# Kernel tuning notes

Measured on AMD Instinct MI355X. Metric: run time of the kernel, lower is better.

## Reference

```python
import jax, jax.numpy as jnp
import numpy as np

# ---------------- geometry constants (from init_kwargs) ----------------
N_PROJ = 96          # cone-beam projections (batch of 2D BP, views of 3D BP)
A2D    = 96          # 2D parallel angles (= detector rows of cone sinogram)
DET2D  = 192         # 2D detector bins   (= detector cols of cone sinogram)
DS2D   = 1.0         # 2D detector spacing
H = 128
W = 128              # intermediate CB_projection image (geom_2d volume)
Zd = 128
Yd = 128
Xd = 128             # reconstruction volume (geometry.volume_shape)
DSO = 500.0          # source-isocenter distance
DSD = 1000.0         # source-detector distance
DU = 3.5
DV = 3.5             # 3D detector spacing (detector grid == H x W image grid)


def _grad_lastdim(x):
    # torch.gradient(x, dim=-1) with unit spacing: central diffs, one-sided edges
    left = x[..., 1:2] - x[..., 0:1]
    mid = (x[..., 2:] - x[..., :-2]) * 0.5
    right = x[..., -1:] - x[..., -2:-1]
    return jnp.concatenate([left, mid, right], axis=-1)


def _image_grid(h, w):
    ys = jnp.arange(h, dtype=jnp.float32) - (h - 1) / 2.0
    xs = jnp.arange(w, dtype=jnp.float32) - (w - 1) / 2.0
    yg, xg = jnp.meshgrid(ys, xs, indexing='ij')  # [h, w]
    return yg, xg


def _weights_3d():
    # Defrise-Clack intermediate-function weighting: cosine of ray angle,
    # w(x,y) = D / sqrt(D^2 + x^2 + y^2) on the intermediate image grid.
    yg, xg = _image_grid(H, W)
    return DSD / jnp.sqrt(DSD * DSD + xg * xg + yg * yg)


def _bp2d(sino):
    # Pixel-driven 2D parallel backprojection, batched over N.
    # sino: [N, A2D, DET2D] -> [N, H, W]
    yg, xg = _image_grid(H, W)
    th = jnp.arange(A2D, dtype=jnp.float32) * (np.pi / A2D)
    s = jnp.cos(th)[:, None, None] * xg + jnp.sin(th)[:, None, None] * yg  # [A,H,W]
    pos = s / DS2D + (DET2D - 1) / 2.0
    i0 = jnp.floor(pos).astype(jnp.int32)
    f = pos - i0
    i1 = i0 + 1
    w0 = jnp.where((i0 >= 0) & (i0 < DET2D), 1.0 - f, 0.0)
    w1 = jnp.where((i1 >= 0) & (i1 < DET2D), f, 0.0)
    i0c = jnp.clip(i0, 0, DET2D - 1)
    i1c = jnp.clip(i1, 0, DET2D - 1)
    aa = jnp.arange(A2D)[:, None, None]  # [A,1,1]
    g0 = sino[:, aa, i0c]  # [N, A, H, W]
    g1 = sino[:, aa, i1c]
    return (g0 * w0 + g1 * w1).sum(axis=1)  # [N, H, W]


def _bp3d(projs):
    # Voxel-driven circular cone-beam backprojection with FDK distance weight.
    # projs: [N_PROJ, H, W] (V=H rows, U=W cols) -> volume [Zd, Yd, Xd]
    zs = jnp.arange(Zd, dtype=jnp.float32) - (Zd - 1) / 2.0
    ys = jnp.arange(Yd, dtype=jnp.float32) - (Yd - 1) / 2.0
    xs = jnp.arange(Xd, dtype=jnp.float32) - (Xd - 1) / 2.0
    zz, yy, xx = jnp.meshgrid(zs, ys, xs, indexing='ij')  # [Z,Y,X]
    betas = jnp.arange(N_PROJ, dtype=jnp.float32) * (2.0 * np.pi / N_PROJ)

    def body(acc, inp):
        beta, proj = inp
        cb, sb = jnp.cos(beta), jnp.sin(beta)
        t = xx * cb + yy * sb          # along central ray
        s = -xx * sb + yy * cb         # transaxial offset
        r = DSO + t                    # source-to-voxel-plane distance
        pu = (DSD * s / r) / DU + (W - 1) / 2.0
        pv = (DSD * zz / r) / DV + (H - 1) / 2.0
        iu0 = jnp.floor(pu).astype(jnp.int32); fu = pu - iu0; iu1 = iu0 + 1
        iv0 = jnp.floor(pv).astype(jnp.int32); fv = pv - iv0; iv1 = iv0 + 1
        mu0 = (iu0 >= 0) & (iu0 < W); mu1 = (iu1 >= 0) & (iu1 < W)
        mv0 = (iv0 >= 0) & (iv0 < H); mv1 = (iv1 >= 0) & (iv1 < H)
        iu0c = jnp.clip(iu0, 0, W - 1); iu1c = jnp.clip(iu1, 0, W - 1)
        iv0c = jnp.clip(iv0, 0, H - 1); iv1c = jnp.clip(iv1, 0, H - 1)
        w00 = jnp.where(mv0 & mu0, (1 - fv) * (1 - fu), 0.0)
        w01 = jnp.where(mv0 & mu1, (1 - fv) * fu, 0.0)
        w10 = jnp.where(mv1 & mu0, fv * (1 - fu), 0.0)
        w11 = jnp.where(mv1 & mu1, fv * fu, 0.0)
        val = (proj[iv0c, iu0c] * w00 + proj[iv0c, iu1c] * w01 +
               proj[iv1c, iu0c] * w10 + proj[iv1c, iu1c] * w11)
        acc = acc + val * (DSD / r) ** 2
        return acc, None

    acc, _ = jax.lax.scan(body, jnp.zeros((Zd, Yd, Xd), jnp.float32), (betas, projs))
    return acc


def setup_inputs() -> dict:
    key = jax.random.key(0)
    k1, k2 = jax.random.split(key)
    sinogram = jax.random.normal(k1, (1, 1, N_PROJ, A2D, DET2D), dtype=jnp.float32)
    weight = jax.random.uniform(k2, (1, N_PROJ, A2D, DET2D), dtype=jnp.float32)
    prelu_weight = jnp.full((1,), 0.25, dtype=jnp.float32)
    return {"sinogram": sinogram, "weight": weight, "prelu_weight": prelu_weight}


def reference(sinogram, weight, prelu_weight):
    ws = sinogram[0] * weight                 # [1, N, A, D]
    deriv = _grad_lastdim(ws)[0]              # [N, A, D]  (squeeze dim 0)
    cb = _bp2d(deriv)                         # [N, H, W]
    weighted_cb = cb * _weights_3d()          # [N, H, W]
    reco = _bp3d(weighted_cb)[None]           # [1, Z, Y, X]
    a = prelu_weight[0]
    return jnp.where(reco >= 0, reco, a * reco)  # PReLU (single parameter)
```

## Files before the change

### kernel.cpp

```cpp
#include <hip/hip_runtime.h>
#include <hip/hip_fp16.h>
#include <math.h>

#define NPROJ 96
#define NANG  96
#define DET   192
#define NPIX  16384
#define SLICE (NANG*DET)

#define KPROJ 285.7142857142857f

__device__ __forceinline__ float frcp(float x) { return __builtin_amdgcn_rcpf(x); }

__device__ __forceinline__ float ffract(float x) {
#if __has_builtin(__builtin_amdgcn_fractf)
    return __builtin_amdgcn_fractf(x);
#else
    return x - floorf(x);
#endif
}

typedef __fp16 h2 __attribute__((ext_vector_type(2)));

__device__ __forceinline__ unsigned pack2(float a, float b) {
    h2 p = __builtin_amdgcn_cvt_pkrtz(a, b);
    return __builtin_bit_cast(unsigned, p);
}
__device__ __forceinline__ h2 as_h2(unsigned u) { return __builtin_bit_cast(h2, u); }

#if __has_builtin(__builtin_amdgcn_fdot2)
#define FDOT2(a, b, c) __builtin_amdgcn_fdot2((a), (b), (c), false)
#else
__device__ __forceinline__ float FDOT2(h2 a, h2 b, float c) {
    return c + (float)a[0] * (float)b[0] + (float)a[1] * (float)b[1];
}
#endif

__global__ __launch_bounds__(192) void k_deriv(const float* __restrict__ sino,
                                               const float* __restrict__ wgt,
                                               unsigned* __restrict__ derivp) {
    __shared__ float row[DET];
    const int r = blockIdx.x;
    const int d = threadIdx.x;
    const int base = r * DET + d;
    row[d] = sino[base] * wgt[base];
    __syncthreads();
    auto grad = [&](int i) -> float {
        i = (i > DET-1) ? DET-1 : i;
        if (i == 0)       return row[1] - row[0];
        if (i == DET-1)   return row[DET-1] - row[DET-2];
        return 0.5f * (row[i+1] - row[i-1]);
    };
    const float g0 = grad(d), g1 = grad(d+1);
    derivp[base] = pack2(g0, g1 - g0);
}

__global__ __launch_bounds__(256) void k_bp2d(const unsigned* __restrict__ derivp,
                                              unsigned* __restrict__ wq_dw) {
    __shared__ float sc[NANG], ss[NANG];
    __shared__ float buf[512];
    const int p   = blockIdx.x;
    const int tid = threadIdx.x;

    if (tid < NANG) {
        float s_, c_;
        sincosf((float)tid * (float)(3.14159265358979323846 / 96.0), &s_, &c_);
        sc[tid] = c_; ss[tid] = s_;
    }

    const int pixbase = blockIdx.y * 512;
    float acc[2], fx[2], fy[2];
    #pragma unroll
    for (int i = 0; i < 2; ++i) {
        const int pix = pixbase + i*256 + tid;
        fx[i] = (float)(pix & 127) - 63.5f;
        fy[i] = (float)(pix >> 7)  - 63.5f;
        acc[i] = 0.0f;
    }
    __syncthreads();

    const unsigned* rowp = derivp + p * SLICE;
    for (int a = 0; a < NANG; ++a, rowp += DET) {
        const float cb = sc[a], sb = ss[a];
        #pragma unroll
        for (int i = 0; i < 2; ++i) {
            const float pos = fmaf(cb, fx[i], fmaf(sb, fy[i], 95.5f));
            const int   i0  = (int)pos;
            const float f   = ffract(pos);
            acc[i] = FDOT2(as_h2(rowp[i0]), as_h2(pack2(1.0f, f)), acc[i]);
        }
    }

    #pragma unroll
    for (int i = 0; i < 2; ++i) {
        const float w = 1000.0f * rsqrtf(1000000.0f + fx[i]*fx[i] + fy[i]*fy[i]);
        buf[i*256 + tid] = acc[i] * w;
    }
    __syncthreads();

    unsigned* sq = wq_dw + p * (NPIX * 4);
    #pragma unroll
    for (int i = 0; i < 2; ++i) {
        const int l   = i*256 + tid;
        const int pix = pixbase + l;
        const int u   = pix & 127;
        const int v   = pix >> 7;
        const float v0 = buf[l];
        const float v1 = (u < 127) ? buf[l + 1] : 0.0f;
        const unsigned pr = pack2(v0, v1 - v0);
        #pragma unroll
        for (int k = 0; k < 4; ++k) {
            const int vb = v - k;
            if (vb >= 0) sq[(((vb << 7) + u) << 2) + k] = pr;
        }
    }
}

__global__ __launch_bounds__(256) void k_bp3d_q(const uint4* __restrict__ wq,
                                                const float* __restrict__ prelu,
                                                float* __restrict__ out) {
    __shared__ float sc[NPROJ], ss[NPROJ];
    const int tid = threadIdx.x;
    const int x   = tid & 127;
    const int y   = (blockIdx.x << 1) | (tid >> 7);
    const int z0  = blockIdx.y << 2;

    if (tid < NPROJ) {
        float s_, c_;
        sincosf((float)tid * (float)(2.0 * 3.14159265358979323846 / 96.0), &s_, &c_);
        sc[tid] = c_; ss[tid] = s_;
    }

    const float fx  = (float)x - 63.5f;
    const float fy  = (float)y - 63.5f;
    const float zlo = (float)z0 - 63.5f;

    float acc[4];
    #pragma unroll
    for (int j = 0; j < 4; ++j) acc[j] = 0.0f;

    __syncthreads();

    const uint4* bb = wq;
    for (int b = 0; b < NPROJ; ++b, bb += NPIX) {
        const float cb    = sc[b], sb = ss[b];
        const float t     = fmaf(fx, cb,  fy * sb);
        const float sdist = fmaf(fy, cb, -fx * sb);
        const float invr  = frcp(500.0f + t);
        const float pu    = fmaf(KPROJ * sdist, invr, 63.5f);
        const int   iu0   = (int)pu;
        const float fu    = ffract(pu);
        float w2 = 1000.0f * invr; w2 *= w2;
        const float Kz    = KPROJ * invr;
        const h2    wuw   = as_h2(pack2(w2, fu * w2));

        #pragma unroll
        for (int pr2 = 0; pr2 < 2; ++pr2) {
            const float pvA = fmaf(Kz, zlo + (float)(2*pr2), 63.5f);
            const float pvB = pvA + Kz;
            const int   ivA = (int)pvA;
            const int   ivB = (int)pvB;
            const float fvA = ffract(pvA);
            const float fvB = ffract(pvB);
            const uint4 q   = bb[(ivA << 7) + iu0];
            const int   d   = ivB - ivA;
            const float tA  = FDOT2(as_h2(q.x), wuw, 0.0f);
            const float bA  = FDOT2(as_h2(q.y), wuw, 0.0f);
            acc[2*pr2]     += fmaf(fvA, bA - tA, tA);
            const unsigned tBv = d ? q.y : q.x;
            const unsigned bBv = d ? q.z : q.y;
            const float tB  = FDOT2(as_h2(tBv), wuw, 0.0f);
            const float bB  = FDOT2(as_h2(bBv), wuw, 0.0f);
            acc[2*pr2 + 1] += fmaf(fvB, bB - tB, tB);
        }
    }

    const float a = prelu[0];
    #pragma unroll
    for (int j = 0; j < 4; ++j) {
        const float v = acc[j];
        out[((z0 + j) << 14) + (y << 7) + x] = (v >= 0.0f) ? v : a * v;
    }
}

extern "C" void kernel_launch(void* const* d_in, const int* in_sizes, int n_in,
                              void* d_out, int out_size, void* d_ws, size_t ws_size,
                              hipStream_t stream) {
    const float* sino  = (const float*)d_in[0];
    const float* wgt   = (const float*)d_in[1];
    const float* prelu = (const float*)d_in[2];
    float* out = (float*)d_out;

    unsigned* wq_dw  = (unsigned*)d_ws;
    unsigned* derivp = wq_dw + (size_t)NPROJ * NPIX * 4;

    k_deriv<<<dim3(NPROJ * NANG), dim3(192), 0, stream>>>(sino, wgt, derivp);
    k_bp2d <<<dim3(NPROJ, 32),    dim3(256), 0, stream>>>(derivp, wq_dw);
    k_bp3d_q<<<dim3(64, 32),      dim3(256), 0, stream>>>((const uint4*)wq_dw, prelu, out);
}
```

Before: 188.0 us.

## Shrink intermediate to 2-row packed layout and do 8 z-voxels per thread

The bp2d output now stores each pixel's data with only two rows (v, v+1) as a uint2, replacing the 4-row uint4 replication. This halves the intermediate buffer and the bytes written and read. In exchange, bp3d issues two 8-byte gathers per z-pair instead of one 16-byte gather plus selects. Each bp3d thread now accumulates 8 z voxels, which halves the grid and amortizes the per-projection geometry math, at the cost of more registers.

```diff
diff --git a/kernel.cpp b/kernel.cpp
--- a/kernel.cpp
+++ b/kernel.cpp
@@ -98,7 +98,7 @@
     }
     __syncthreads();
 
-    unsigned* sq = wq_dw + p * (NPIX * 4);
+    unsigned* sq = wq_dw + p * (NPIX * 2);
     #pragma unroll
     for (int i = 0; i < 2; ++i) {
         const int l   = i*256 + tid;
@@ -108,22 +108,19 @@
         const float v0 = buf[l];
         const float v1 = (u < 127) ? buf[l + 1] : 0.0f;
         const unsigned pr = pack2(v0, v1 - v0);
-        #pragma unroll
-        for (int k = 0; k < 4; ++k) {
-            const int vb = v - k;
-            if (vb >= 0) sq[(((vb << 7) + u) << 2) + k] = pr;
-        }
+        sq[(((v << 7) + u) << 1)] = pr;
+        if (v >= 1) sq[((((v - 1) << 7) + u) << 1) + 1] = pr;
     }
 }
 
-__global__ __launch_bounds__(256) void k_bp3d_q(const uint4* __restrict__ wq,
+__global__ __launch_bounds__(256) void k_bp3d_p(const uint2* __restrict__ wp,
                                                 const float* __restrict__ prelu,
                                                 float* __restrict__ out) {
     __shared__ float sc[NPROJ], ss[NPROJ];
     const int tid = threadIdx.x;
     const int x   = tid & 127;
     const int y   = (blockIdx.x << 1) | (tid >> 7);
-    const int z0  = blockIdx.y << 2;
+    const int z0  = blockIdx.y << 3;
 
     if (tid < NPROJ) {
         float s_, c_;
@@ -133,16 +130,18 @@
 
     const float fx  = (float)x - 63.5f;
     const float fy  = (float)y - 63.5f;
-    const float zlo = (float)z0 - 63.5f;
+    float za[4];
+    #pragma unroll
+    for (int j = 0; j < 4; ++j) za[j] = (float)z0 - 63.5f + (float)(2*j);
 
-    float acc[4];
+    float acc[8];
     #pragma unroll
-    for (int j = 0; j < 4; ++j) acc[j] = 0.0f;
+    for (int j = 0; j < 8; ++j) acc[j] = 0.0f;
 
     __syncthreads();
 
-    const uint4* bb = wq;
-    for (int b = 0; b < NPROJ; ++b, bb += NPIX) {
+    const char* bbc = (const char*)wp;
+    for (int b = 0; b < NPROJ; ++b, bbc += (size_t)NPIX * sizeof(uint2)) {
         const float cb    = sc[b], sb = ss[b];
         const float t     = fmaf(fx, cb,  fy * sb);
         const float sdist = fmaf(fy, cb, -fx * sb);
@@ -153,31 +152,30 @@
         float w2 = 1000.0f * invr; w2 *= w2;
         const float Kz    = KPROJ * invr;
         const h2    wuw   = as_h2(pack2(w2, fu * w2));
+        const unsigned ub = ((unsigned)iu0) << 3;
 
         #pragma unroll
-        for (int pr2 = 0; pr2 < 2; ++pr2) {
-            const float pvA = fmaf(Kz, zlo + (float)(2*pr2), 63.5f);
+        for (int pr2 = 0; pr2 < 4; ++pr2) {
+            const float pvA = fmaf(Kz, za[pr2], 63.5f);
             const float pvB = pvA + Kz;
             const int   ivA = (int)pvA;
             const int   ivB = (int)pvB;
             const float fvA = ffract(pvA);
             const float fvB = ffract(pvB);
-            const uint4 q   = bb[(ivA << 7) + iu0];
-            const int   d   = ivB - ivA;
-            const float tA  = FDOT2(as_h2(q.x), wuw, 0.0f);
-            const float bA  = FDOT2(as_h2(q.y), wuw, 0.0f);
+            const uint2 qA  = *(const uint2*)(bbc + ((((unsigned)ivA) << 10) + ub));
+            const uint2 qB  = *(const uint2*)(bbc + ((((unsigned)ivB) << 10) + ub));
+            const float tA  = FDOT2(as_h2(qA.x), wuw, 0.0f);
+            const float bA  = FDOT2(as_h2(qA.y), wuw, 0.0f);
             acc[2*pr2]     += fmaf(fvA, bA - tA, tA);
-            const unsigned tBv = d ? q.y : q.x;
-            const unsigned bBv = d ? q.z : q.y;
-            const float tB  = FDOT2(as_h2(tBv), wuw, 0.0f);
-            const float bB  = FDOT2(as_h2(bBv), wuw, 0.0f);
+            const float tB  = FDOT2(as_h2(qB.x), wuw, 0.0f);
+            const float bB  = FDOT2(as_h2(qB.y), wuw, 0.0f);
             acc[2*pr2 + 1] += fmaf(fvB, bB - tB, tB);
         }
     }
 
     const float a = prelu[0];
     #pragma unroll
-    for (int j = 0; j < 4; ++j) {
+    for (int j = 0; j < 8; ++j) {
         const float v = acc[j];
         out[((z0 + j) << 14) + (y << 7) + x] = (v >= 0.0f) ? v : a * v;
     }
@@ -192,9 +190,9 @@
     float* out = (float*)d_out;
 
     unsigned* wq_dw  = (unsigned*)d_ws;
-    unsigned* derivp = wq_dw + (size_t)NPROJ * NPIX * 4;
+    unsigned* derivp = wq_dw + (size_t)NPROJ * NPIX * 2;
 
     k_deriv<<<dim3(NPROJ * NANG), dim3(192), 0, stream>>>(sino, wgt, derivp);
     k_bp2d <<<dim3(NPROJ, 32),    dim3(256), 0, stream>>>(derivp, wq_dw);
-    k_bp3d_q<<<dim3(64, 32),      dim3(256), 0, stream>>>((const uint4*)wq_dw, prelu, out);
+    k_bp3d_p<<<dim3(64, 16),      dim3(256), 0, stream>>>((const uint2*)wq_dw, prelu, out);
 }
```

Measured after the change: 212.0 us. 12.7% more time.

## Precompute per-projection 3D backprojection geometry table and crop unused detector rows

Applied to the files above, without the earlier changes.

The per-(projection, x, y) geometry of the 3D backprojection no longer runs in every z-block. It is now computed once in the 2D backprojection kernel and stored as a packed table holding the fp16 weights, iu0 packed into Kz's low mantissa bits, and Kz. The 3D kernel loads this table with a software prefetch and issues both z-pair gathers up front, so it skips the trig, reciprocal and fract work that was repeated 32 times. The intermediate buffer keeps only detector rows 16..111, which shrinks the writes and the footprint. Trade-offs: an extra 12 MB table read per z-block, a slight loss of Kz precision, and the row crop assumes projections never fall outside that range.

```diff
diff --git a/kernel.cpp b/kernel.cpp
--- a/kernel.cpp
+++ b/kernel.cpp
@@ -7,6 +7,10 @@
 #define DET   192
 #define NPIX  16384
 #define SLICE (NANG*DET)
+
+#define WQROW0   16
+#define WQROWS   96
+#define WQSLICEB (WQROWS*128*16)
 
 #define KPROJ 285.7142857142857f
 
@@ -56,7 +60,8 @@
 }
 
 __global__ __launch_bounds__(256) void k_bp2d(const unsigned* __restrict__ derivp,
-                                              unsigned* __restrict__ wq_dw) {
+                                              unsigned* __restrict__ wq_dw,
+                                              uint2* __restrict__ tbl) {
     __shared__ float sc[NANG], ss[NANG];
     __shared__ float buf[512];
     const int p   = blockIdx.x;
@@ -67,6 +72,9 @@
         sincosf((float)tid * (float)(3.14159265358979323846 / 96.0), &s_, &c_);
         sc[tid] = c_; ss[tid] = s_;
     }
+
+    float sb2, cb2;
+    sincosf((float)p * (float)(2.0 * 3.14159265358979323846 / 96.0), &sb2, &cb2);
 
     const int pixbase = blockIdx.y * 512;
     float acc[2], fx[2], fy[2];
@@ -98,7 +106,8 @@
     }
     __syncthreads();
 
-    unsigned* sq = wq_dw + p * (NPIX * 4);
+    unsigned* sq = wq_dw + p * (WQROWS * 128 * 4);
+    uint2*    tp = tbl   + p * NPIX;
     #pragma unroll
     for (int i = 0; i < 2; ++i) {
         const int l   = i*256 + tid;
@@ -111,68 +120,88 @@
         #pragma unroll
         for (int k = 0; k < 4; ++k) {
             const int vb = v - k;
-            if (vb >= 0) sq[(((vb << 7) + u) << 2) + k] = pr;
-        }
-    }
-}
-
-__global__ __launch_bounds__(256) void k_bp3d_q(const uint4* __restrict__ wq,
-                                                const float* __restrict__ prelu,
-                                                float* __restrict__ out) {
-    __shared__ float sc[NPROJ], ss[NPROJ];
+            if (vb >= WQROW0 && vb < WQROW0 + WQROWS)
+                sq[(((vb - WQROW0) << 7) + u) << 2 | k] = pr;
+        }
+        const float t3   = fmaf(fx[i], cb2,  fy[i] * sb2);
+        const float sd3  = fmaf(fy[i], cb2, -fx[i] * sb2);
+        const float invr = frcp(500.0f + t3);
+        const float pu   = fmaf(KPROJ * sd3, invr, 63.5f);
+        const int   iu0  = (int)pu;
+        const float fu   = ffract(pu);
+        float w2 = 1000.0f * invr; w2 *= w2;
+        const float Kz   = KPROJ * invr;
+        const unsigned kzi = (__builtin_bit_cast(unsigned, Kz) & ~127u) | (unsigned)iu0;
+        uint2 e; e.x = pack2(w2, fu * w2); e.y = kzi;
+        tp[pix] = e;
+    }
+}
+
+__global__ __launch_bounds__(256, 8) void k_bp3d_t(const unsigned char* __restrict__ wq,
+                                                   const uint2* __restrict__ tbl,
+                                                   const float* __restrict__ prelu,
+                                                   float* __restrict__ out) {
     const int tid = threadIdx.x;
     const int x   = tid & 127;
     const int y   = (blockIdx.x << 1) | (tid >> 7);
     const int z0  = blockIdx.y << 2;
-
-    if (tid < NPROJ) {
-        float s_, c_;
-        sincosf((float)tid * (float)(2.0 * 3.14159265358979323846 / 96.0), &s_, &c_);
-        sc[tid] = c_; ss[tid] = s_;
-    }
-
-    const float fx  = (float)x - 63.5f;
-    const float fy  = (float)y - 63.5f;
+    const int pix = (y << 7) + x;
+
     const float zlo = (float)z0 - 63.5f;
 
     float acc[4];
     #pragma unroll
     for (int j = 0; j < 4; ++j) acc[j] = 0.0f;
 
-    __syncthreads();
-
-    const uint4* bb = wq;
-    for (int b = 0; b < NPROJ; ++b, bb += NPIX) {
-        const float cb    = sc[b], sb = ss[b];
-        const float t     = fmaf(fx, cb,  fy * sb);
-        const float sdist = fmaf(fy, cb, -fx * sb);
-        const float invr  = frcp(500.0f + t);
-        const float pu    = fmaf(KPROJ * sdist, invr, 63.5f);
-        const int   iu0   = (int)pu;
-        const float fu    = ffract(pu);
-        float w2 = 1000.0f * invr; w2 *= w2;
-        const float Kz    = KPROJ * invr;
-        const h2    wuw   = as_h2(pack2(w2, fu * w2));
-
-        #pragma unroll
-        for (int pr2 = 0; pr2 < 2; ++pr2) {
-            const float pvA = fmaf(Kz, zlo + (float)(2*pr2), 63.5f);
-            const float pvB = pvA + Kz;
-            const int   ivA = (int)pvA;
-            const int   ivB = (int)pvB;
-            const float fvA = ffract(pvA);
-            const float fvB = ffract(pvB);
-            const uint4 q   = bb[(ivA << 7) + iu0];
-            const int   d   = ivB - ivA;
-            const float tA  = FDOT2(as_h2(q.x), wuw, 0.0f);
-            const float bA  = FDOT2(as_h2(q.y), wuw, 0.0f);
-            acc[2*pr2]     += fmaf(fvA, bA - tA, tA);
-            const unsigned tBv = d ? q.y : q.x;
-            const unsigned bBv = d ? q.z : q.y;
-            const float tB  = FDOT2(as_h2(tBv), wuw, 0.0f);
-            const float bB  = FDOT2(as_h2(bBv), wuw, 0.0f);
-            acc[2*pr2 + 1] += fmaf(fvB, bB - tB, tB);
-        }
+    const uint2* tp = tbl + pix;
+    const unsigned char* sp = wq;
+
+    uint2 Tc = *tp; tp += NPIX;
+
+    for (int b = 0; b < NPROJ; ++b, tp += NPIX, sp += WQSLICEB) {
+        const uint2 Tn = *tp;
+        const h2    wuw = as_h2(Tc.x);
+        const int   iu0 = (int)(Tc.y & 127u);
+        const float Kz  = __builtin_bit_cast(float, Tc.y & ~127u);
+        const int   ub2 = (iu0 << 4) - (WQROW0 << 11);
+
+        const float pvA0 = fmaf(Kz, zlo, 63.5f);
+        const float pvB0 = pvA0 + Kz;
+        const int   ivA0 = (int)pvA0;
+        const int   d0   = (int)pvB0 - ivA0;
+        const float fvA0 = ffract(pvA0);
+        const float fvB0 = ffract(pvB0);
+        const uint4 q0   = *(const uint4*)(sp + ((ivA0 << 11) + ub2));
+
+        const float pvA1 = fmaf(Kz, zlo + 2.0f, 63.5f);
+        const float pvB1 = pvA1 + Kz;
+        const int   ivA1 = (int)pvA1;
+        const int   d1   = (int)pvB1 - ivA1;
+        const float fvA1 = ffract(pvA1);
+        const float fvB1 = ffract(pvB1);
+        const uint4 q1   = *(const uint4*)(sp + ((ivA1 << 11) + ub2));
+
+        {
+            const float tA = FDOT2(as_h2(q0.x), wuw, 0.0f);
+            const float bA = FDOT2(as_h2(q0.y), wuw, 0.0f);
+            acc[0] += fmaf(fvA0, bA - tA, tA);
+            const unsigned tBv = d0 ? q0.y : q0.x;
+            const unsigned bBv = d0 ? q0.z : q0.y;
+            const float tB = FDOT2(as_h2(tBv), wuw, 0.0f);
+            const float bB = FDOT2(as_h2(bBv), wuw, 0.0f);
+            acc[1] += fmaf(fvB0, bB - tB, tB);
+        }
+        {
+            const float tA = FDOT2(as_h2(q1.x), wuw, 0.0f);
+            const float bA = FDOT2(as_h2(q1.y), wuw, 0.0f);
+            acc[2] += fmaf(fvA1, bA - tA, tA);
+            const unsigned tBv = d1 ? q1.y : q1.x;
+            const unsigned bBv = d1 ? q1.z : q1.y;
+            const float tB = FDOT2(as_h2(tBv), wuw, 0.0f);
+            const float bB = FDOT2(as_h2(bBv), wuw, 0.0f);
+            acc[3] += fmaf(fvB1, bB - tB, tB);
+        }
+        Tc = Tn;
     }
 
     const float a = prelu[0];
@@ -191,10 +220,13 @@
     const float* prelu = (const float*)d_in[2];
     float* out = (float*)d_out;
 
-    unsigned* wq_dw  = (unsigned*)d_ws;
-    unsigned* derivp = wq_dw + (size_t)NPROJ * NPIX * 4;
-
-    k_deriv<<<dim3(NPROJ * NANG), dim3(192), 0, stream>>>(sino, wgt, derivp);
-    k_bp2d <<<dim3(NPROJ, 32),    dim3(256), 0, stream>>>(derivp, wq_dw);
-    k_bp3d_q<<<dim3(64, 32),      dim3(256), 0, stream>>>((const uint4*)wq_dw, prelu, out);
-}
+    unsigned char* wsb = (unsigned char*)d_ws;
+    unsigned* wq_dw  = (unsigned*)wsb;
+    uint2*    tbl    = (uint2*)(wsb + (size_t)NPROJ * WQSLICEB);
+    unsigned* derivp = (unsigned*)(wsb + (size_t)NPROJ * WQSLICEB
+                                       + (size_t)NPROJ * NPIX * 8);
+
+    k_deriv <<<dim3(NPROJ * NANG), dim3(192), 0, stream>>>(sino, wgt, derivp);
+    k_bp2d  <<<dim3(NPROJ, 32),    dim3(256), 0, stream>>>(derivp, wq_dw, tbl);
+    k_bp3d_t<<<dim3(64, 32),       dim3(256), 0, stream>>>((const unsigned char*)wq_dw, tbl, prelu, out);
+}
```

Measured after the change: 184.2 us. -2.0%, faster.
